# Kernel tuning notes

Measured on AMD Instinct MI355X. Metric: run time of the kernel, lower is better.

The kernel has to match this reference:

```python
import jax, jax.numpy as jnp
import numpy as np

# Fixed molemap hierarchy: leaf groups under level-2 nodes 65..72
GROUPS = [(0, 7), (7, 30), (30, 48), (48, 53), (53, 58), (58, 59), (59, 62), (62, 65)]
GROUP_SIZES = [b - a for a, b in GROUPS]
# group index of each leaf (which of nodes 65..72 is its parent)
GIDX = np.repeat(np.arange(8), GROUP_SIZES)
# top branch of each leaf: 0 -> node 73 (leaves 0..52), 1 -> node 74 (leaves 53..64)
TIDX = (np.arange(65) >= 53).astype(np.int32)


def _forward(x):
    # x: [N, 65] leaf logits
    N = x.shape[0]
    # leaf-level probs: softmax of leaf logits within each sibling group (children of 65..72)
    leaf_probs = jnp.concatenate(
        [jax.nn.softmax(x[:, a:b], axis=-1) for a, b in GROUPS], axis=-1
    )  # [N, 65]
    # level-2 node logits = mean of their leaf logits (nodes 65..72)
    means = jnp.stack([x[:, a:b].mean(axis=-1) for a, b in GROUPS], axis=-1)  # [N, 8]
    # level-1 node logits = mean over all leaves beneath (node 73: leaves 0..52, node 74: 53..64)
    m_top = jnp.stack([x[:, :53].mean(axis=-1), x[:, 53:].mean(axis=-1)], axis=-1)  # [N, 2]
    p_top = jax.nn.softmax(m_top, axis=-1)  # [N, 2] -> nodes 73, 74
    # level-2 probs: softmax among siblings (65..68 under 73, 69..72 under 74)
    p_lvl2 = jnp.concatenate(
        [jax.nn.softmax(means[:, :4], axis=-1), jax.nn.softmax(means[:, 4:], axis=-1)],
        axis=-1,
    )  # [N, 8] -> nodes 65..72
    # node_probs layout: [leaves 0..64 | nodes 65..72 | nodes 73..74 | root 75 (=1)]
    node_probs = jnp.concatenate(
        [leaf_probs, p_lvl2, p_top, jnp.ones((N, 1), dtype=x.dtype)], axis=-1
    )  # [N, 76]
    # root-to-leaf path product: p(root)=1 * p(level1) * p(level2) * p(leaf)
    leaf_path_probs = leaf_probs * p_lvl2[:, GIDX] * p_top[:, TIDX]  # [N, 65]
    return leaf_path_probs, node_probs


def setup_inputs() -> dict:
    key = jax.random.key(0)
    x = jax.random.normal(key, (524288, 65), dtype=jnp.float32)
    return {"x": x}


def reference(x):
    return _forward(x)
```

## Files before the change

### kernel.cpp

```cpp
#include <hip/hip_runtime.h>
#include <hip/hip_bf16.h>
#include <math.h>


#define NLEAF 65
#define NNODE 76
#define ROWS  128
#define TPB   128
#define NSTRIDE 77

#define NF   (ROWS * NLEAF)
#define NF4  (NF / 4)
#define NQ4  (ROWS * (NNODE/4))

__global__ __launch_bounds__(TPB) void hier_molemap_kernel(
    const float* __restrict__ x,
    float* __restrict__ out_leaf,
    float* __restrict__ out_node,
    int N)
{
    __shared__ float lds[ROWS * NSTRIDE];

    const int tid  = threadIdx.x;
    const int row0 = blockIdx.x * ROWS;
    if (row0 >= N) return;
    const int R    = min(ROWS, N - row0);
    const bool full = (R == ROWS);

    if (full) {
        const float4* __restrict__ src4 = (const float4*)(x + (size_t)row0 * NLEAF);
        float4* lds4 = (float4*)lds;
#pragma unroll
        for (int i = 0; i <= NF4 / TPB; ++i) {
            int idx = tid + i * TPB;
            if (idx < NF4) lds4[idx] = src4[idx];
        }
    } else {
        const float* __restrict__ src = x + (size_t)row0 * NLEAF;
        for (int i = tid; i < R * NLEAF; i += TPB) lds[i] = src[i];
    }
    __syncthreads();

    float v[NLEAF];
    float p2[8];
    float pt0 = 0.0f, pt1 = 0.0f;

    constexpr int ga[8] = {0, 7, 30, 48, 53, 58, 59, 62};
    constexpr int gb[8] = {7, 30, 48, 53, 58, 59, 62, 65};

    if (tid < R) {
        const float* __restrict__ r = lds + tid * NLEAF;
#pragma unroll
        for (int i = 0; i < NLEAF; ++i) v[i] = r[i];

        float gsum[8], means[8];
#pragma unroll
        for (int g = 0; g < 8; ++g) {
            float mx = -INFINITY, sx = 0.0f;
#pragma unroll
            for (int i = ga[g]; i < gb[g]; ++i) { mx = fmaxf(mx, v[i]); sx += v[i]; }
            gsum[g]  = sx;
            means[g] = sx * (1.0f / (float)(gb[g] - ga[g]));
            float denom = 0.0f;
#pragma unroll
            for (int i = ga[g]; i < gb[g]; ++i) {
                float e = __expf(v[i] - mx);
                v[i] = e;
                denom += e;
            }
            float inv = 1.0f / denom;
#pragma unroll
            for (int i = ga[g]; i < gb[g]; ++i) v[i] *= inv;
        }

        float m0 = (gsum[0] + gsum[1] + gsum[2] + gsum[3]) * (1.0f / 53.0f);
        float m1 = (gsum[4] + gsum[5] + gsum[6] + gsum[7]) * (1.0f / 12.0f);
        float mt = fmaxf(m0, m1);
        float e0 = __expf(m0 - mt), e1 = __expf(m1 - mt);
        float invt = 1.0f / (e0 + e1);
        pt0 = e0 * invt; pt1 = e1 * invt;

        float mxa = fmaxf(fmaxf(means[0], means[1]), fmaxf(means[2], means[3]));
        float sa = 0.0f;
#pragma unroll
        for (int g = 0; g < 4; ++g) { p2[g] = __expf(means[g] - mxa); sa += p2[g]; }
        float inva = 1.0f / sa;
#pragma unroll
        for (int g = 0; g < 4; ++g) p2[g] *= inva;

        float mxb = fmaxf(fmaxf(means[4], means[5]), fmaxf(means[6], means[7]));
        float sb = 0.0f;
#pragma unroll
        for (int g = 4; g < 8; ++g) { p2[g] = __expf(means[g] - mxb); sb += p2[g]; }
        float invb = 1.0f / sb;
#pragma unroll
        for (int g = 4; g < 8; ++g) p2[g] *= invb;

        float* __restrict__ w = lds + tid * NLEAF;
#pragma unroll
        for (int g = 0; g < 8; ++g) {
            float f = p2[g] * ((g < 4) ? pt0 : pt1);
#pragma unroll
            for (int i = ga[g]; i < gb[g]; ++i) w[i] = v[i] * f;
        }
    }
    __syncthreads();

    if (full) {
        float4* __restrict__ dst4 = (float4*)(out_leaf + (size_t)row0 * NLEAF);
        const float4* lds4 = (const float4*)lds;
#pragma unroll
        for (int i = 0; i <= NF4 / TPB; ++i) {
            int idx = tid + i * TPB;
            if (idx < NF4) dst4[idx] = lds4[idx];
        }
    } else {
        float* __restrict__ dst = out_leaf + (size_t)row0 * NLEAF;
        for (int i = tid; i < R * NLEAF; i += TPB) dst[i] = lds[i];
    }
    __syncthreads();

    if (tid < R) {
        float* __restrict__ nr = lds + tid * NSTRIDE;
#pragma unroll
        for (int i = 0; i < NLEAF; ++i) nr[i] = v[i];
#pragma unroll
        for (int g = 0; g < 8; ++g) nr[NLEAF + g] = p2[g];
        nr[73] = pt0;
        nr[74] = pt1;
        nr[75] = 1.0f;
    }
    __syncthreads();

    if (full) {
        float4* __restrict__ dst4 = (float4*)(out_node + (size_t)row0 * NNODE);
#pragma unroll
        for (int i = 0; i < NQ4 / TPB; ++i) {
            int q = tid + i * TPB;
            int r = q / (NNODE / 4);
            int c = q - r * (NNODE / 4);
            const float* s = lds + r * NSTRIDE + c * 4;
            float4 val;
            val.x = s[0]; val.y = s[1]; val.z = s[2]; val.w = s[3];
            dst4[q] = val;
        }
    } else {
        float* __restrict__ dst = out_node + (size_t)row0 * NNODE;
        for (int j = tid; j < R * NNODE; j += TPB) {
            int r = j / NNODE;
            int c = j - r * NNODE;
            dst[j] = lds[r * NSTRIDE + c];
        }
    }
}

extern "C" void kernel_launch(void* const* d_in, const int* in_sizes, int n_in,
                              void* d_out, int out_size, void* d_ws, size_t ws_size,
                              hipStream_t stream) {
    const float* x = (const float*)d_in[0];
    int N = in_sizes[0] / NLEAF;

    float* out_leaf = (float*)d_out;
    float* out_node = (float*)d_out + (size_t)N * NLEAF;

    int grid = (N + ROWS - 1) / ROWS;
    hier_molemap_kernel<<<grid, TPB, 0, stream>>>(x, out_leaf, out_node, N);
}
```

Baseline: 393.4 us.

## Use single-wave blocks with async global-to-LDS loads and packed node staging

Shrinks each block to one 64-thread wavefront handling 64 rows, so the later block barriers become plain LDS waitcnt instructions. The input tile is loaded with global_load_lds async copies that bypass registers. The node-output staging switches from a padded 77-float stride to a packed 76-float layout written with float4 stores, so the final copy is a straight float4 LDS-to-global move without per-element index math. This trades block-level parallelism and padding for fewer barriers and instructions. The async LDS copy relies on the wave-uniform LDS base addressing of that builtin, and the packed stride may cause more LDS bank conflicts.

```diff
diff --git a/kernel.cpp b/kernel.cpp
--- a/kernel.cpp
+++ b/kernel.cpp
@@ -1,25 +1,32 @@
 #include <hip/hip_runtime.h>
-#include <hip/hip_bf16.h>
 #include <math.h>
 
 
 #define NLEAF 65
 #define NNODE 76
-#define ROWS  128
-#define TPB   128
-#define NSTRIDE 77
+#define ROWS  64
+#define TPB   64
 
-#define NF   (ROWS * NLEAF)
-#define NF4  (NF / 4)
-#define NQ4  (ROWS * (NNODE/4))
+#define NF4    ((ROWS * NLEAF) / 4)
+#define NQ4    ((ROWS * NNODE) / 4)
+#define FULL_A (NF4 / TPB)
+#define TAIL_A (NF4 - FULL_A * TPB)
+#define FULL_E (NQ4 / TPB)
 
-__global__ __launch_bounds__(TPB) void hier_molemap_kernel(
+__device__ __forceinline__ void async_copy16(const float4* g, float4* l) {
+    __builtin_amdgcn_global_load_lds(
+        (const __attribute__((address_space(1))) void*)g,
+        (__attribute__((address_space(3))) void*)l,
+        16, 0, 0);
+}
+
+__global__ __launch_bounds__(TPB, 2) void hier_molemap_kernel(
     const float* __restrict__ x,
     float* __restrict__ out_leaf,
     float* __restrict__ out_node,
     int N)
 {
-    __shared__ float lds[ROWS * NSTRIDE];
+    __shared__ float lds[ROWS * NNODE];
 
     const int tid  = threadIdx.x;
     const int row0 = blockIdx.x * ROWS;
@@ -31,10 +38,10 @@
         const float4* __restrict__ src4 = (const float4*)(x + (size_t)row0 * NLEAF);
         float4* lds4 = (float4*)lds;
 #pragma unroll
-        for (int i = 0; i <= NF4 / TPB; ++i) {
-            int idx = tid + i * TPB;
-            if (idx < NF4) lds4[idx] = src4[idx];
-        }
+        for (int i = 0; i < FULL_A; ++i)
+            async_copy16(src4 + tid + i * TPB, lds4 + tid + i * TPB);
+        if (tid < TAIL_A)
+            async_copy16(src4 + tid + FULL_A * TPB, lds4 + tid + FULL_A * TPB);
     } else {
         const float* __restrict__ src = x + (size_t)row0 * NLEAF;
         for (int i = tid; i < R * NLEAF; i += TPB) lds[i] = src[i];
@@ -104,53 +111,57 @@
             for (int i = ga[g]; i < gb[g]; ++i) w[i] = v[i] * f;
         }
     }
-    __syncthreads();
+    asm volatile("s_waitcnt lgkmcnt(0)" ::: "memory");
 
     if (full) {
         float4* __restrict__ dst4 = (float4*)(out_leaf + (size_t)row0 * NLEAF);
         const float4* lds4 = (const float4*)lds;
 #pragma unroll
-        for (int i = 0; i <= NF4 / TPB; ++i) {
+        for (int i = 0; i < FULL_A; ++i) {
             int idx = tid + i * TPB;
-            if (idx < NF4) dst4[idx] = lds4[idx];
+            dst4[idx] = lds4[idx];
+        }
+        if (tid < TAIL_A) {
+            int idx = tid + FULL_A * TPB;
+            dst4[idx] = lds4[idx];
         }
     } else {
         float* __restrict__ dst = out_leaf + (size_t)row0 * NLEAF;
         for (int i = tid; i < R * NLEAF; i += TPB) dst[i] = lds[i];
     }
-    __syncthreads();
+    asm volatile("s_waitcnt lgkmcnt(0)" ::: "memory");
 
     if (tid < R) {
-        float* __restrict__ nr = lds + tid * NSTRIDE;
+        float4* __restrict__ nrow4 = (float4*)lds + tid * (NNODE / 4);
 #pragma unroll
-        for (int i = 0; i < NLEAF; ++i) nr[i] = v[i];
-#pragma unroll
-        for (int g = 0; g < 8; ++g) nr[NLEAF + g] = p2[g];
-        nr[73] = pt0;
-        nr[74] = pt1;
-        nr[75] = 1.0f;
+        for (int c = 0; c < 16; ++c) {
+            float4 t;
+            t.x = v[4 * c + 0];
+            t.y = v[4 * c + 1];
+            t.z = v[4 * c + 2];
+            t.w = v[4 * c + 3];
+            nrow4[c] = t;
+        }
+        float4 t16; t16.x = v[64];  t16.y = p2[0]; t16.z = p2[1]; t16.w = p2[2];
+        nrow4[16] = t16;
+        float4 t17; t17.x = p2[3];  t17.y = p2[4]; t17.z = p2[5]; t17.w = p2[6];
+        nrow4[17] = t17;
+        float4 t18; t18.x = p2[7];  t18.y = pt0;   t18.z = pt1;   t18.w = 1.0f;
+        nrow4[18] = t18;
     }
-    __syncthreads();
+    asm volatile("s_waitcnt lgkmcnt(0)" ::: "memory");
 
     if (full) {
         float4* __restrict__ dst4 = (float4*)(out_node + (size_t)row0 * NNODE);
+        const float4* lds4 = (const float4*)lds;
 #pragma unroll
-        for (int i = 0; i < NQ4 / TPB; ++i) {
+        for (int i = 0; i < FULL_E; ++i) {
             int q = tid + i * TPB;
-            int r = q / (NNODE / 4);
-            int c = q - r * (NNODE / 4);
-            const float* s = lds + r * NSTRIDE + c * 4;
-            float4 val;
-            val.x = s[0]; val.y = s[1]; val.z = s[2]; val.w = s[3];
-            dst4[q] = val;
+            dst4[q] = lds4[q];
         }
     } else {
         float* __restrict__ dst = out_node + (size_t)row0 * NNODE;
-        for (int j = tid; j < R * NNODE; j += TPB) {
-            int r = j / NNODE;
-            int c = j - r * NNODE;
-            dst[j] = lds[r * NSTRIDE + c];
-        }
+        for (int j = tid; j < R * NNODE; j += TPB) dst[j] = lds[j];
     }
 }
 
```

Result: no change. 386.3 us (-1.8%).
